# Kernel tuning notes

Measured on AMD Instinct MI355X. Metric: run time of the kernel, lower is better.

## Reference

```python
import jax, jax.numpy as jnp
import numpy as np

N = 50000      # nodes
E = 800000     # edges (avg degree 16)
DIM = 256      # in_channels == heads * out_channels
H = 8          # heads
C = DIM // H   # per-head out_channels = 32
EDGE_DIM = 2
NEG_SLOPE = 0.2


def setup_inputs() -> dict:
    key = jax.random.key(0)
    ks = jax.random.split(key, 8)
    x = jax.random.normal(ks[0], (N, DIM), dtype=jnp.float32)
    edge_index = jax.random.randint(ks[1], (2, E), 0, N, dtype=jnp.int32)
    edge_attr = jax.random.normal(ks[2], (E, EDGE_DIM), dtype=jnp.float32)
    s = 1.0 / np.sqrt(DIM)
    W_l = jax.random.normal(ks[3], (DIM, H * C), dtype=jnp.float32) * s   # lin_l (src)
    W_r = jax.random.normal(ks[4], (DIM, H * C), dtype=jnp.float32) * s   # lin_r (dst)
    W_e = jax.random.normal(ks[5], (EDGE_DIM, H * C), dtype=jnp.float32) * (1.0 / np.sqrt(EDGE_DIM))
    att = jax.random.normal(ks[6], (H, C), dtype=jnp.float32) * s         # attention vector a
    bias = jnp.zeros((H * C,), dtype=jnp.float32)
    return {"x": x, "edge_index": edge_index, "edge_attr": edge_attr,
            "W_l": W_l, "W_r": W_r, "W_e": W_e, "att": att, "bias": bias}


def reference(x, edge_index, edge_attr, W_l, W_r, W_e, att, bias):
    src, dst = edge_index[0], edge_index[1]
    # --- add self loops; fill_value='mean' => scatter-mean of incoming edge_attr per node ---
    attr_sum = jax.ops.segment_sum(edge_attr, dst, num_segments=N)          # [N, 2]
    cnt = jax.ops.segment_sum(jnp.ones((edge_attr.shape[0], 1), edge_attr.dtype), dst, num_segments=N)
    loop_attr = attr_sum / jnp.maximum(cnt, 1.0)                             # [N, 2], 0 for isolated nodes
    idx = jnp.arange(N, dtype=src.dtype)
    src_a = jnp.concatenate([src, idx])                                      # [E+N]
    dst_a = jnp.concatenate([dst, idx])
    ea = jnp.concatenate([edge_attr, loop_attr], axis=0)                     # [E+N, 2]
    # --- GATv2: project src/dst/edge features ---
    x_l = (x @ W_l).reshape(N, H, C)
    x_r = (x @ W_r).reshape(N, H, C)
    e_e = (ea @ W_e).reshape(-1, H, C)                                       # [E+N, H, C]
    m = x_l[src_a] + x_r[dst_a] + e_e                                        # [E+N, H, C]
    score = jnp.einsum('ehc,hc->eh', jax.nn.leaky_relu(m, NEG_SLOPE), att)   # [E+N, H]
    # --- segment softmax over incoming edges of each dst (self loop guarantees >=1 edge) ---
    smax = jax.ops.segment_max(score, dst_a, num_segments=N)                 # [N, H]
    ex = jnp.exp(score - smax[dst_a])
    denom = jax.ops.segment_sum(ex, dst_a, num_segments=N)                   # [N, H]
    alpha = ex / denom[dst_a]                                                # [E+N, H]
    # --- weighted scatter-add of src messages ---
    out = jax.ops.segment_sum(alpha[..., None] * x_l[src_a], dst_a, num_segments=N)  # [N, H, C]
    return out.reshape(N, H * C) + bias
```

## Files before the change

### kernel.cpp

```cpp
#include <hip/hip_runtime.h>
#include <hip/hip_bf16.h>

#define NN 50000
#define NPAD 53248
#define EE 800000
#define DIM 256
#define NEG_SLOPE 0.2f
#define LOG2E 1.44269504088896f

#define GEMM_BLOCKS 1564
#define FILL_BLOCKS 3125
#define CNT_BLOCKS  3125
#define CVT_BLOCKS  12500
#define WT_BLOCKS   512

typedef __attribute__((ext_vector_type(8))) short short8;
typedef __attribute__((ext_vector_type(4))) float f32x4;
typedef __attribute__((ext_vector_type(2))) float v2f;

__device__ __forceinline__ unsigned short f2bf(float f) {
    unsigned u = __float_as_uint(f);
    unsigned r = (u + 0x7fffu + ((u >> 16) & 1u)) >> 16;
    return (unsigned short)r;
}
__device__ __forceinline__ float bf2f(unsigned short h) {
    return __uint_as_float(((unsigned)h) << 16);
}
__device__ __forceinline__ float u2f_lo(unsigned u) {
    return __uint_as_float(u << 16);
}
__device__ __forceinline__ float u2f_hi(unsigned u) {
    return __uint_as_float(u & 0xffff0000u);
}

__device__ __forceinline__ float red8(float s) {
    int t;
    t = __builtin_amdgcn_update_dpp(0, __float_as_int(s), 0xB1, 0xF, 0xF, true);
    s += __int_as_float(t);
    t = __builtin_amdgcn_update_dpp(0, __float_as_int(s), 0x4E, 0xF, 0xF, true);
    s += __int_as_float(t);
    t = __builtin_amdgcn_update_dpp(0, __float_as_int(s), 0x141, 0xF, 0xF, true);
    s += __int_as_float(t);
    return s;
}

__global__ __launch_bounds__(256) void k_prep_count(
    const float* __restrict__ x, const float* __restrict__ Wl,
    const float* __restrict__ Wr, const int* __restrict__ ei,
    unsigned short* __restrict__ xb, unsigned short* __restrict__ wt,
    int* __restrict__ cnt, int* __restrict__ rank)
{
    int b = blockIdx.x;
    if (b < CNT_BLOCKS) {
        int e = b * 256 + threadIdx.x;
        if (e < EE) {
            int dst = ei[EE + e];
            rank[e] = atomicAdd(&cnt[dst], 1);
        }
    } else if (b < CNT_BLOCKS + CVT_BLOCKS) {
        int i = ((b - CNT_BLOCKS) * 256 + threadIdx.x) * 4;
        float4 v = *(const float4*)(x + i);
        ushort4 o;
        o.x = f2bf(v.x); o.y = f2bf(v.y); o.z = f2bf(v.z); o.w = f2bf(v.w);
        *(ushort4*)(xb + i) = o;
    } else {
        int idx = (b - CNT_BLOCKS - CVT_BLOCKS) * 256 + threadIdx.x;
        int n = idx >> 8, k = idx & 255;
        float v = (n < 256) ? Wl[k * 256 + n] : Wr[k * 256 + (n - 256)];
        wt[idx] = f2bf(v);
    }
}

__global__ __launch_bounds__(1024) void k_scan(
    const int* __restrict__ cnt, int* __restrict__ row_start)
{
    __shared__ int wsum[16];
    int tid = threadIdx.x, lane = tid & 63, wid = tid >> 6;
    int4 v[13];
#pragma unroll
    for (int p = 0; p < 13; ++p)
        v[p] = *(const int4*)(cnt + p * 4096 + tid * 4);
    int carry = 0;
#pragma unroll
    for (int p = 0; p < 13; ++p) {
        int4 vv = v[p];
        int tsum = vv.x + vv.y + vv.z + vv.w;
        int s = tsum;
#pragma unroll
        for (int off = 1; off < 64; off <<= 1) {
            int t = __shfl_up(s, off, 64);
            if (lane >= off) s += t;
        }
        if (lane == 63) wsum[wid] = s;
        __syncthreads();
        int wpre = 0, tot = 0;
#pragma unroll
        for (int w = 0; w < 16; ++w) {
            int xv = wsum[w];
            tot += xv;
            if (w < wid) wpre += xv;
        }
        int ex = carry + wpre + (s - tsum);
        int4 o;
        o.x = ex;
        o.y = o.x + vv.x;
        o.z = o.y + vv.y;
        o.w = o.z + vv.z;
        *(int4*)(row_start + p * 4096 + tid * 4) = o;
        carry += tot;
        __syncthreads();
    }
}

__global__ __launch_bounds__(256) void k_gemm_fill(
    const unsigned short* __restrict__ xb, const unsigned short* __restrict__ wt,
    const int* __restrict__ ei, const float* __restrict__ ea,
    const int* __restrict__ row_start, const int* __restrict__ rank,
    unsigned short* __restrict__ xlr, uint2* __restrict__ edge_rec)
{
    __shared__ short sAB[8192];
    int tid = threadIdx.x;

    if (blockIdx.x >= GEMM_BLOCKS) {
        int e = (blockIdx.x - GEMM_BLOCKS) * 256 + tid;
        if (e < EE) {
            int src = ei[e];
            int dst = ei[EE + e];
            float2 a = *(const float2*)(ea + 2 * e);
            int pos = row_start[dst] + rank[e];
            unsigned packed = ((unsigned)f2bf(a.y) << 16) | f2bf(a.x);
            edge_rec[pos] = make_uint2((unsigned)src, packed);
        }
        return;
    }

    int wid = tid >> 6, lane = tid & 63;
    int mt = blockIdx.x >> 2, nt = blockIdx.x & 3;
    int mBase = mt * 128, nBase = nt * 128;
    int wm = (wid & 1) * 64, wn = (wid >> 1) * 64;
    int q = lane >> 4, mh = lane & 15;

    f32x4 acc[4][4];
#pragma unroll
    for (int i = 0; i < 4; ++i)
#pragma unroll
        for (int j = 0; j < 4; ++j)
            acc[i][j] = (f32x4){0.f, 0.f, 0.f, 0.f};

    int aoff[4], boff[4];
#pragma unroll
    for (int f = 0; f < 4; ++f) {
        int r  = wm + f * 16 + mh;
        aoff[f] = (r * 4 + (q ^ (r & 3))) * 8;
        int nl = wn + f * 16 + mh;
        boff[f] = 4096 + (nl * 4 + (q ^ (nl & 3))) * 8;
    }

    for (int k0 = 0; k0 < 256; k0 += 32) {
        __syncthreads();
#pragma unroll
        for (int it = 0; it < 4; ++it) {
            int L = it * 256 + tid;
            const unsigned short* g;
            if (L < 512) {
                int r  = L >> 2;
                int qq = (L & 3) ^ (r & 3);
                int grow = mBase + r;
                if (grow > NN - 1) grow = NN - 1;
                g = xb + (size_t)grow * 256 + k0 + qq * 8;
            } else {
                int LB = L - 512;
                int nl = LB >> 2;
                int qq = (LB & 3) ^ (nl & 3);
                g = wt + (size_t)(nBase + nl) * 256 + k0 + qq * 8;
            }
            short* lp = sAB + (it * 256 + wid * 64) * 8;
            __builtin_amdgcn_global_load_lds(
                (const __attribute__((address_space(1))) void*)g,
                (__attribute__((address_space(3))) void*)lp, 16, 0, 0);
        }
        __syncthreads();

        short8 af[4], bfr[4];
#pragma unroll
        for (int f = 0; f < 4; ++f) af[f]  = *(const short8*)(sAB + aoff[f]);
#pragma unroll
        for (int f = 0; f < 4; ++f) bfr[f] = *(const short8*)(sAB + boff[f]);
#pragma unroll
        for (int i = 0; i < 4; ++i)
#pragma unroll
            for (int j = 0; j < 4; ++j)
                acc[i][j] = __builtin_amdgcn_mfma_f32_16x16x32_bf16(
                    af[i], bfr[j], acc[i][j], 0, 0, 0);
    }

#pragma unroll
    for (int i = 0; i < 4; ++i)
#pragma unroll
        for (int j = 0; j < 4; ++j)
#pragma unroll
            for (int r = 0; r < 4; ++r) {
                int row = mBase + wm + i * 16 + q * 4 + r;
                if (row < NN) {
                    int col = nBase + wn + j * 16 + mh;
                    xlr[(size_t)row * 512 + col] = f2bf(acc[i][j][r]);
                }
            }
}

__global__ __launch_bounds__(256) void k_attn(
    const unsigned short* __restrict__ xlr, const int* __restrict__ row_start,
    const uint2* __restrict__ edge_rec, const float* __restrict__ W_e,
    const float* __restrict__ att, const float* __restrict__ bias,
    float* __restrict__ out)
{
    int n = __builtin_amdgcn_readfirstlane(blockIdx.x * 4 + (threadIdx.x >> 6));
    if (n >= NN) return;
    int lane = threadIdx.x & 63;
    int j = lane * 4;

    const unsigned short* nrow = xlr + ((size_t)n << 9);
    uint2 xru = *(const uint2*)(nrow + 256 + j);
    v2f xr01 = {u2f_lo(xru.x), u2f_hi(xru.x)};
    v2f xr23 = {u2f_lo(xru.y), u2f_hi(xru.y)};
    float4 av = *(const float4*)(att + j);
    v2f att01 = {av.x * LOG2E, av.y * LOG2E};
    v2f att23 = {av.z * LOG2E, av.w * LOG2E};
    float4 w0v = *(const float4*)(W_e + j);
    float4 w1v = *(const float4*)(W_e + 256 + j);
    v2f we0_01 = {w0v.x, w0v.y}, we0_23 = {w0v.z, w0v.w};
    v2f we1_01 = {w1v.x, w1v.y}, we1_23 = {w1v.z, w1v.w};
    const v2f sl2 = {NEG_SLOPE, NEG_SLOPE};

    int rs = __builtin_amdgcn_readfirstlane(row_start[n]);
    int cn = __builtin_amdgcn_readfirstlane(row_start[n + 1]) - rs;

    float D = 0.0f, la0 = 0.0f, la1 = 0.0f;
    v2f acc01 = {0.f, 0.f}, acc23 = {0.f, 0.f};

    auto body = [&](uint2 ru, float a0, float a1) {
        v2f xl01 = {u2f_lo(ru.x), u2f_hi(ru.x)};
        v2f xl23 = {u2f_lo(ru.y), u2f_hi(ru.y)};
        v2f a0v = {a0, a0}, a1v = {a1, a1};
        v2f m01 = xl01 + xr01;
        v2f m23 = xl23 + xr23;
        m01 = __builtin_elementwise_fma(a0v, we0_01, m01);
        m23 = __builtin_elementwise_fma(a0v, we0_23, m23);
        m01 = __builtin_elementwise_fma(a1v, we1_01, m01);
        m23 = __builtin_elementwise_fma(a1v, we1_23, m23);
        v2f t01 = __builtin_elementwise_max(m01, m01 * sl2);
        v2f t23 = __builtin_elementwise_max(m23, m23 * sl2);
        v2f sv = t01 * att01;
        sv = __builtin_elementwise_fma(t23, att23, sv);
        float s = sv.x + sv.y;
        s = red8(s);
        float w = __builtin_amdgcn_exp2f(s);
        D += w;
        v2f wv = {w, w};
        acc01 = __builtin_elementwise_fma(wv, xl01, acc01);
        acc23 = __builtin_elementwise_fma(wv, xl23, acc23);
    };

    int done = 0;
    while (done < cn) {
        int m = cn - done; if (m > 64) m = 64;
        int ridx = rs + done + lane;
        if (ridx > EE + 63) ridx = EE + 63;
        uint2 rc = edge_rec[ridx];
        int rcx = (int)rc.x, rca = (int)rc.y;

        auto gat = [&](int k) -> uint2 {
            unsigned sidx = (unsigned)__builtin_amdgcn_readlane(rcx, k);
            return *(const uint2*)(xlr + ((size_t)sidx << 9) + j);
        };
        auto proc = [&](uint2 xu, int k) {
            unsigned pk = (unsigned)__builtin_amdgcn_readlane(rca, k);
            float a0 = __uint_as_float(pk << 16);
            float a1 = __uint_as_float(pk & 0xffff0000u);
            la0 += a0; la1 += a1;
            body(xu, a0, a1);
        };

        uint2 x0 = gat(0), x1 = gat(1), x2 = gat(2), x3 = gat(3);
        for (int i = 0; i < m; i += 4) {
            proc(x0, i);
            if (i + 4 < m) x0 = gat(i + 4);
            if (i + 1 < m) { proc(x1, i + 1); if (i + 5 < m) x1 = gat(i + 5); }
            if (i + 2 < m) { proc(x2, i + 2); if (i + 6 < m) x2 = gat(i + 6); }
            if (i + 3 < m) { proc(x3, i + 3); if (i + 7 < m) x3 = gat(i + 7); }
        }
        done += m;
    }

    float invc = 1.0f / fmaxf((float)cn, 1.0f);
    uint2 xs = *(const uint2*)(nrow + j);
    body(xs, la0 * invc, la1 * invc);

    float invD = 1.0f / D;
    float4 b4 = *(const float4*)(bias + j);
    float4 o;
    o.x = fmaf(acc01.x, invD, b4.x);
    o.y = fmaf(acc01.y, invD, b4.y);
    o.z = fmaf(acc23.x, invD, b4.z);
    o.w = fmaf(acc23.y, invD, b4.w);
    *(float4*)(out + (size_t)n * 256 + j) = o;
}

extern "C" void kernel_launch(void* const* d_in, const int* in_sizes, int n_in,
                              void* d_out, int out_size, void* d_ws, size_t ws_size,
                              hipStream_t stream)
{
    const float* x    = (const float*)d_in[0];
    const int*   ei   = (const int*)  d_in[1];
    const float* ea   = (const float*)d_in[2];
    const float* Wl   = (const float*)d_in[3];
    const float* Wr   = (const float*)d_in[4];
    const float* We   = (const float*)d_in[5];
    const float* att  = (const float*)d_in[6];
    const float* bias = (const float*)d_in[7];
    float* out = (float*)d_out;

    char* ws = (char*)d_ws;
    size_t off = 0;
    unsigned short* xlr = (unsigned short*)(ws + off); off += (size_t)NN * 512 * 2;
    unsigned short* xb  = (unsigned short*)(ws + off); off += (size_t)NN * 256 * 2;
    uint2*  edge_rec    = (uint2*)(ws + off);          off += (size_t)(EE + 64) * 8;
    int*    rank        = (int*)(ws + off);            off += (size_t)EE * 4;
    unsigned short* wt  = (unsigned short*)(ws + off); off += (size_t)512 * 256 * 2;
    int*    cnt         = (int*)(ws + off);            off += (size_t)NPAD * 4;
    int*    row_st      = (int*)(ws + off);            off += (size_t)NPAD * 4;

    hipMemsetAsync(cnt, 0, NPAD * sizeof(int), stream);
    hipMemsetAsync(edge_rec + EE, 0, 64 * sizeof(uint2), stream);

    k_prep_count<<<CNT_BLOCKS + CVT_BLOCKS + WT_BLOCKS, 256, 0, stream>>>(
        x, Wl, Wr, ei, xb, wt, cnt, rank);
    k_scan      <<<1, 1024, 0, stream>>>(cnt, row_st);
    k_gemm_fill <<<GEMM_BLOCKS + FILL_BLOCKS, 256, 0, stream>>>(
        xb, wt, ei, ea, row_st, rank, xlr, edge_rec);
    k_attn      <<<12500, 256, 0, stream>>>(
        xlr, row_st, edge_rec, We, att, bias, out);
}
```

Before: 276.6 us.

## Split xl/xr into separate arrays, remap GEMM blocks per XCD, merge memsets

Stores the source and destination projections in two separate 256-wide bf16 arrays instead of one interleaved 512-wide buffer. The gathers in the attention kernel then touch a compact 25.6MB table, which should fit better in cache. GEMM workgroups are remapped so that consecutive tiles land on the same XCD, which should improve L2 reuse of A rows. The two memsets are merged into one by placing cnt right after edge_rec's padding.

```diff
diff --git a/kernel.cpp b/kernel.cpp
--- a/kernel.cpp
+++ b/kernel.cpp
@@ -116,7 +116,8 @@
     const unsigned short* __restrict__ xb, const unsigned short* __restrict__ wt,
     const int* __restrict__ ei, const float* __restrict__ ea,
     const int* __restrict__ row_start, const int* __restrict__ rank,
-    unsigned short* __restrict__ xlr, uint2* __restrict__ edge_rec)
+    unsigned short* __restrict__ xl, unsigned short* __restrict__ xr,
+    uint2* __restrict__ edge_rec)
 {
     __shared__ short sAB[8192];
     int tid = threadIdx.x;
@@ -134,11 +135,17 @@
         return;
     }
 
+    int bid = blockIdx.x;
+    const int q = GEMM_BLOCKS / 8, r = GEMM_BLOCKS % 8;
+    int xcd = bid & 7, kk = bid >> 3;
+    int wg = (xcd < r) ? xcd * (q + 1) + kk
+                       : r * (q + 1) + (xcd - r) * q + kk;
+
     int wid = tid >> 6, lane = tid & 63;
-    int mt = blockIdx.x >> 2, nt = blockIdx.x & 3;
+    int mt = wg >> 2, nt = wg & 3;
     int mBase = mt * 128, nBase = nt * 128;
     int wm = (wid & 1) * 64, wn = (wid >> 1) * 64;
-    int q = lane >> 4, mh = lane & 15;
+    int qq4 = lane >> 4, mh = lane & 15;
 
     f32x4 acc[4][4];
 #pragma unroll
@@ -150,10 +157,10 @@
     int aoff[4], boff[4];
 #pragma unroll
     for (int f = 0; f < 4; ++f) {
-        int r  = wm + f * 16 + mh;
-        aoff[f] = (r * 4 + (q ^ (r & 3))) * 8;
+        int rr = wm + f * 16 + mh;
+        aoff[f] = (rr * 4 + (qq4 ^ (rr & 3))) * 8;
         int nl = wn + f * 16 + mh;
-        boff[f] = 4096 + (nl * 4 + (q ^ (nl & 3))) * 8;
+        boff[f] = 4096 + (nl * 4 + (qq4 ^ (nl & 3))) * 8;
     }
 
     for (int k0 = 0; k0 < 256; k0 += 32) {
@@ -163,16 +170,16 @@
             int L = it * 256 + tid;
             const unsigned short* g;
             if (L < 512) {
-                int r  = L >> 2;
-                int qq = (L & 3) ^ (r & 3);
-                int grow = mBase + r;
+                int rr = L >> 2;
+                int q2 = (L & 3) ^ (rr & 3);
+                int grow = mBase + rr;
                 if (grow > NN - 1) grow = NN - 1;
-                g = xb + (size_t)grow * 256 + k0 + qq * 8;
+                g = xb + (size_t)grow * 256 + k0 + q2 * 8;
             } else {
                 int LB = L - 512;
                 int nl = LB >> 2;
-                int qq = (LB & 3) ^ (nl & 3);
-                g = wt + (size_t)(nBase + nl) * 256 + k0 + qq * 8;
+                int q2 = (LB & 3) ^ (nl & 3);
+                g = wt + (size_t)(nBase + nl) * 256 + k0 + q2 * 8;
             }
             short* lp = sAB + (it * 256 + wid * 64) * 8;
             __builtin_amdgcn_global_load_lds(
@@ -194,33 +201,34 @@
                     af[i], bfr[j], acc[i][j], 0, 0, 0);
     }
 
+    unsigned short* cb = (nt < 2) ? xl : xr;
+    int chalf = (nt & 1) * 128;
 #pragma unroll
     for (int i = 0; i < 4; ++i)
 #pragma unroll
         for (int j = 0; j < 4; ++j)
 #pragma unroll
-            for (int r = 0; r < 4; ++r) {
-                int row = mBase + wm + i * 16 + q * 4 + r;
+            for (int rr = 0; rr < 4; ++rr) {
+                int row = mBase + wm + i * 16 + qq4 * 4 + rr;
                 if (row < NN) {
-                    int col = nBase + wn + j * 16 + mh;
-                    xlr[(size_t)row * 512 + col] = f2bf(acc[i][j][r]);
+                    int col = chalf + wn + j * 16 + mh;
+                    cb[(size_t)row * 256 + col] = f2bf(acc[i][j][rr]);
                 }
             }
 }
 
 __global__ __launch_bounds__(256) void k_attn(
-    const unsigned short* __restrict__ xlr, const int* __restrict__ row_start,
-    const uint2* __restrict__ edge_rec, const float* __restrict__ W_e,
-    const float* __restrict__ att, const float* __restrict__ bias,
-    float* __restrict__ out)
+    const unsigned short* __restrict__ xl, const unsigned short* __restrict__ xr,
+    const int* __restrict__ row_start, const uint2* __restrict__ edge_rec,
+    const float* __restrict__ W_e, const float* __restrict__ att,
+    const float* __restrict__ bias, float* __restrict__ out)
 {
     int n = __builtin_amdgcn_readfirstlane(blockIdx.x * 4 + (threadIdx.x >> 6));
     if (n >= NN) return;
     int lane = threadIdx.x & 63;
     int j = lane * 4;
 
-    const unsigned short* nrow = xlr + ((size_t)n << 9);
-    uint2 xru = *(const uint2*)(nrow + 256 + j);
+    uint2 xru = *(const uint2*)(xr + ((size_t)n << 8) + j);
     v2f xr01 = {u2f_lo(xru.x), u2f_hi(xru.x)};
     v2f xr23 = {u2f_lo(xru.y), u2f_hi(xru.y)};
     float4 av = *(const float4*)(att + j);
@@ -271,7 +279,7 @@
 
         auto gat = [&](int k) -> uint2 {
             unsigned sidx = (unsigned)__builtin_amdgcn_readlane(rcx, k);
-            return *(const uint2*)(xlr + ((size_t)sidx << 9) + j);
+            return *(const uint2*)(xl + ((size_t)sidx << 8) + j);
         };
         auto proc = [&](uint2 xu, int k) {
             unsigned pk = (unsigned)__builtin_amdgcn_readlane(rca, k);
@@ -293,7 +301,7 @@
     }
 
     float invc = 1.0f / fmaxf((float)cn, 1.0f);
-    uint2 xs = *(const uint2*)(nrow + j);
+    uint2 xs = *(const uint2*)(xl + ((size_t)n << 8) + j);
     body(xs, la0 * invc, la1 * invc);
 
     float invD = 1.0f / D;
@@ -322,22 +330,22 @@
 
     char* ws = (char*)d_ws;
     size_t off = 0;
-    unsigned short* xlr = (unsigned short*)(ws + off); off += (size_t)NN * 512 * 2;
-    unsigned short* xb  = (unsigned short*)(ws + off); off += (size_t)NN * 256 * 2;
-    uint2*  edge_rec    = (uint2*)(ws + off);          off += (size_t)(EE + 64) * 8;
-    int*    rank        = (int*)(ws + off);            off += (size_t)EE * 4;
-    unsigned short* wt  = (unsigned short*)(ws + off); off += (size_t)512 * 256 * 2;
-    int*    cnt         = (int*)(ws + off);            off += (size_t)NPAD * 4;
-    int*    row_st      = (int*)(ws + off);            off += (size_t)NPAD * 4;
-
-    hipMemsetAsync(cnt, 0, NPAD * sizeof(int), stream);
-    hipMemsetAsync(edge_rec + EE, 0, 64 * sizeof(uint2), stream);
+    unsigned short* xl = (unsigned short*)(ws + off); off += (size_t)NN * 256 * 2;
+    unsigned short* xr = (unsigned short*)(ws + off); off += (size_t)NN * 256 * 2;
+    unsigned short* xb = (unsigned short*)(ws + off); off += (size_t)NN * 256 * 2;
+    uint2*  edge_rec   = (uint2*)(ws + off);          off += (size_t)(EE + 64) * 8;
+    int*    cnt        = (int*)(ws + off);            off += (size_t)NPAD * 4;
+    int*    row_st     = (int*)(ws + off);            off += (size_t)NPAD * 4;
+    int*    rank       = (int*)(ws + off);            off += (size_t)EE * 4;
+    unsigned short* wt = (unsigned short*)(ws + off); off += (size_t)512 * 256 * 2;
+
+    hipMemsetAsync(edge_rec + EE, 0, 64 * sizeof(uint2) + NPAD * sizeof(int), stream);
 
     k_prep_count<<<CNT_BLOCKS + CVT_BLOCKS + WT_BLOCKS, 256, 0, stream>>>(
         x, Wl, Wr, ei, xb, wt, cnt, rank);
     k_scan      <<<1, 1024, 0, stream>>>(cnt, row_st);
     k_gemm_fill <<<GEMM_BLOCKS + FILL_BLOCKS, 256, 0, stream>>>(
-        xb, wt, ei, ea, row_st, rank, xlr, edge_rec);
+        xb, wt, ei, ea, row_st, rank, xl, xr, edge_rec);
     k_attn      <<<12500, 256, 0, stream>>>(
-        xlr, row_st, edge_rec, We, att, bias, out);
-}
+        xl, xr, row_st, edge_rec, We, att, bias, out);
+}
```

Result: faster. 268.9 us (-2.8%).
